# Kernel tuning notes

Measured on AMD Instinct MI355X. Metric: run time of the kernel, lower is better.

Reference implementation:

```python
import jax, jax.numpy as jnp
import numpy as np

DT = 0.01
B = 2097152
STATE_DIM, LATENT_DIM, INPUT_DIM = 3, 4, 3
TOTAL = STATE_DIM + LATENT_DIM  # 7
HID_L, HID_B = 64, 32


def setup_inputs() -> dict:
    key = jax.random.key(0)
    ks = jax.random.split(key, 16)
    def w(k, shape, fan_in):
        return (jax.random.normal(k, shape, dtype=jnp.float32) / np.sqrt(fan_in)).astype(jnp.float32)
    return {
        "state": jax.random.normal(ks[0], (B, TOTAL), dtype=jnp.float32),
        "u": jax.random.normal(ks[1], (B, INPUT_DIM), dtype=jnp.float32),
        # linear physics prior: s_dot = s@A.T + u@Bm.T ; y_phys = s@C.T
        "A": w(ks[2], (STATE_DIM, STATE_DIM), STATE_DIM),
        "Bm": w(ks[3], (STATE_DIM, INPUT_DIM), INPUT_DIM),
        "C": w(ks[4], (STATE_DIM, STATE_DIM), STATE_DIM),
        # z_gate: Linear(10 -> 7) + sigmoid
        "Wz": w(ks[5], (TOTAL, TOTAL + INPUT_DIM), TOTAL + INPUT_DIM),
        "bz": jnp.full((TOTAL,), 2.0, dtype=jnp.float32),
        # latent_dyn: Linear(10 -> 64) tanh Linear(64 -> 4)
        "W1": w(ks[6], (HID_L, TOTAL + INPUT_DIM), TOTAL + INPUT_DIM),
        "b1": jnp.zeros((HID_L,), dtype=jnp.float32),
        "W2": w(ks[7], (LATENT_DIM, HID_L), HID_L),
        "b2": jnp.zeros((LATENT_DIM,), dtype=jnp.float32),
        # 3 branches stacked: Linear(6 -> 32) tanh Linear(32 -> 1)
        "Wb1": w(ks[8], (3, HID_B, STATE_DIM + INPUT_DIM), STATE_DIM + INPUT_DIM),
        "bb1": jnp.zeros((3, HID_B), dtype=jnp.float32),
        "Wb2": w(ks[9], (3, HID_B), HID_B),
        "bb2": jnp.zeros((3,), dtype=jnp.float32),
    }


def reference(state, u, A, Bm, C, Wz, bz, W1, b1, W2, b2, Wb1, bb1, Wb2, bb2):
    s = state[:, :STATE_DIM]          # [B,3]
    latent = state[:, STATE_DIM:]     # [B,4]
    # physics prior
    s_dot_phys = s @ A.T + u @ Bm.T   # [B,3]
    y_phys = s @ C.T                  # [B,3]
    s_phys_next = s + DT * s_dot_phys
    su = jnp.concatenate([state, u], axis=1)  # [B,10]
    # latent dynamics
    latent_dot = jnp.tanh(su @ W1.T + b1) @ W2.T + b2   # [B,4]
    latent_next = latent + DT * latent_dot
    candidate = jnp.concatenate([s_phys_next, latent_next], axis=1)  # [B,7]
    # update gate
    z = jax.nn.sigmoid(su @ Wz.T + bz)                  # [B,7]
    next_state = z * candidate + (1.0 - z) * state
    # residual branch heads (vectorized over the 3 heads)
    branch_in = jnp.concatenate([s, u], axis=1)         # [B,6]
    h = jnp.tanh(jnp.einsum('bi,khi->bkh', branch_in, Wb1) + bb1)  # [B,3,32]
    residuals = jnp.einsum('bkh,kh->bk', h, Wb2) + bb2  # [B,3]
    y = y_phys + residuals
    return (next_state, y)
```

## Files before the change

kernel.cpp:

```cpp
#include <hip/hip_runtime.h>
#include <stdint.h>


#define DT_C  0.01f
#define NROWS 2097152
#define LOG2E 1.4426950408889634f
#define TBL_H   0.03125f
#define INV_H   32.0f
#define INV_H2  16.0f
#define TBL_C   256.0f
#define TBL_MAX 511.999f

typedef __fp16 h2 __attribute__((ext_vector_type(2)));

__device__ __forceinline__ h2 pkrtz(float a, float b) {
    return __builtin_amdgcn_cvt_pkrtz(a, b);
}

#if __has_builtin(__builtin_amdgcn_fdot2)
__device__ __forceinline__ float fdot2(h2 a, h2 b, float c) {
    return __builtin_amdgcn_fdot2(a, b, c, false);
}
#else
__device__ __forceinline__ float fdot2(h2 a, h2 b, float c) {
    return fmaf((float)a[0], (float)b[0], fmaf((float)a[1], (float)b[1], c));
}
#endif

__device__ __forceinline__ float tanh_ref(float x) {
    float e = __builtin_amdgcn_exp2f(x * (2.0f * LOG2E));
    return 1.0f - 2.0f * __builtin_amdgcn_rcpf(1.0f + e);
}

__device__ __forceinline__ float fract_f(float x) {
#if __has_builtin(__builtin_amdgcn_fractf)
    return __builtin_amdgcn_fractf(x);
#else
    return x - truncf(x);
#endif
}

__device__ __forceinline__ float med3f(float x, float lo, float hi) {
#if __has_builtin(__builtin_amdgcn_fmed3f)
    return __builtin_amdgcn_fmed3f(x, lo, hi);
#else
    return fminf(fmaxf(x, lo), hi);
#endif
}

__device__ __forceinline__ float tanh_lut(float t, const float2* lut) {
    float tc = med3f(t, 0.0f, TBL_MAX);
    float fr = fract_f(tc);
    int   i  = (int)tc;
    float2 e = lut[i];
    return fmaf(e.y, fr, e.x);
}

#define W1P_OFF   0
#define WZP_OFF   320
#define WB1P_OFF  355
#define W2P_OFF   643
#define PHYSP_OFF 771
#define CP_OFF    780
#define B1S_OFF   786
#define BZS_OFF   850
#define BB1S_OFF  857

__device__ __forceinline__ uint32_t pack2(float a, float b) {
    h2 v = pkrtz(a, b);
    uint32_t u; __builtin_memcpy(&u, &v, 4); return u;
}

__global__ void prep_kernel(const float* __restrict__ A, const float* __restrict__ Bm,
                            const float* __restrict__ C, const float* __restrict__ Wz,
                            const float* __restrict__ bz, const float* __restrict__ W1,
                            const float* __restrict__ b1, const float* __restrict__ Wb1,
                            const float* __restrict__ bb1, const float* __restrict__ W2,
                            uint32_t* __restrict__ ws)
{
    const int tid = blockIdx.x * blockDim.x + threadIdx.x;
    const int nt = gridDim.x * blockDim.x;
    float* wsf = (float*)ws;

    for (int i = tid; i < 320; i += nt) {
        int h = i / 5, j = i % 5;
        ws[W1P_OFF + i] = pack2(W1[h*10 + 2*j] * INV_H, W1[h*10 + 2*j + 1] * INV_H);
    }
    for (int i = tid; i < 35; i += nt) {
        int r = i / 5, j = i % 5;
        ws[WZP_OFF + i] = pack2(Wz[r*10 + 2*j] * INV_H2, Wz[r*10 + 2*j + 1] * INV_H2);
    }
    for (int i = tid; i < 288; i += nt) {
        int row = i / 3, j = i % 3;
        ws[WB1P_OFF + i] = pack2(Wb1[row*6 + 2*j] * INV_H, Wb1[row*6 + 2*j + 1] * INV_H);
    }
    for (int i = tid; i < 128; i += nt) {
        int k = i / 32, j = i % 32;
        ws[W2P_OFF + i] = pack2(W2[k*64 + 2*j], W2[k*64 + 2*j + 1]);
    }
    for (int i = tid; i < 9; i += nt) {
        int r = i / 3, j = i % 3;
        float a, b;
        if (j == 0) { a = A[r*3+0];  b = A[r*3+1];  }
        else if (j == 1) { a = A[r*3+2];  b = Bm[r*3+0]; }
        else { a = Bm[r*3+1]; b = Bm[r*3+2]; }
        ws[PHYSP_OFF + i] = pack2(a, b);
    }
    for (int i = tid; i < 6; i += nt) {
        int r = i / 2, j = i % 2;
        float a = (j == 0) ? C[r*3+0] : C[r*3+2];
        float b = (j == 0) ? C[r*3+1] : 0.0f;
        ws[CP_OFF + i] = pack2(a, b);
    }
    for (int i = tid; i < 64; i += nt) wsf[B1S_OFF + i] = fmaf(b1[i], INV_H, TBL_C);
    for (int i = tid; i < 7;  i += nt) wsf[BZS_OFF + i] = fmaf(bz[i], INV_H2, TBL_C);
    for (int i = tid; i < 96; i += nt) wsf[BB1S_OFF + i] = fmaf(bb1[i], INV_H, TBL_C);
}

__global__ __launch_bounds__(256) void phygru_kernel(
    const float* __restrict__ state, const float* __restrict__ u,
    const uint32_t* __restrict__ ws, const float* __restrict__ b2,
    const float* __restrict__ Wb2,   const float* __restrict__ bb2,
    float* __restrict__ out)
{
    __shared__ float2 lut[512];
    {
        const int t0 = threadIdx.x;
        #pragma unroll
        for (int r = 0; r < 2; ++r) {
            int j = t0 + r * 256;
            float x  = (j - 256) * TBL_H;
            float v0 = tanh_ref(x);
            float v1 = tanh_ref(x + TBL_H);
            lut[j] = make_float2(v0, v1 - v0);
        }
    }
    __syncthreads();

    const int row = blockIdx.x * blockDim.x + threadIdx.x;

    const h2* W1p  = (const h2*)(ws + W1P_OFF);
    const h2* Wzp  = (const h2*)(ws + WZP_OFF);
    const h2* Wb1p = (const h2*)(ws + WB1P_OFF);
    const h2* W2p  = (const h2*)(ws + W2P_OFF);
    const h2* Pp   = (const h2*)(ws + PHYSP_OFF);
    const h2* Cp   = (const h2*)(ws + CP_OFF);
    const float* wsf  = (const float*)ws;
    const float* b1s  = wsf + B1S_OFF;
    const float* bzs  = wsf + BZS_OFF;
    const float* bb1s = wsf + BB1S_OFF;

    float st[7];
    #pragma unroll
    for (int i = 0; i < 7; ++i) st[i] = state[row * 7 + i];
    float uu[3];
    #pragma unroll
    for (int i = 0; i < 3; ++i) uu[i] = u[row * 3 + i];

    h2 suh[5];
    suh[0] = pkrtz(st[0], st[1]);
    suh[1] = pkrtz(st[2], st[3]);
    suh[2] = pkrtz(st[4], st[5]);
    suh[3] = pkrtz(st[6], uu[0]);
    suh[4] = pkrtz(uu[1], uu[2]);
    h2 bih[3];
    bih[0] = suh[0];
    bih[1] = pkrtz(st[2], uu[0]);
    bih[2] = suh[4];

    float sp[3], yp[3];
    #pragma unroll
    for (int r = 0; r < 3; ++r) {
        float sd = fdot2(Pp[r*3+0], bih[0],
                   fdot2(Pp[r*3+1], bih[1],
                   fdot2(Pp[r*3+2], bih[2], 0.0f)));
        sp[r] = fmaf(DT_C, sd, st[r]);
        yp[r] = fdot2(Cp[r*2+0], bih[0], fdot2(Cp[r*2+1], bih[1], 0.0f));
    }

    float ld0 = b2[0], ld1 = b2[1], ld2 = b2[2], ld3 = b2[3];
    #pragma unroll
    for (int hp = 0; hp < 32; ++hp) {
        const int h0 = 2 * hp, h1 = 2 * hp + 1;
        float a0 = b1s[h0], a1 = b1s[h1];
        #pragma unroll
        for (int j = 0; j < 5; ++j) {
            a0 = fdot2(W1p[h0*5 + j], suh[j], a0);
            a1 = fdot2(W1p[h1*5 + j], suh[j], a1);
        }
        h2 th = pkrtz(tanh_lut(a0, lut), tanh_lut(a1, lut));
        ld0 = fdot2(W2p[0*32 + hp], th, ld0);
        ld1 = fdot2(W2p[1*32 + hp], th, ld1);
        ld2 = fdot2(W2p[2*32 + hp], th, ld2);
        ld3 = fdot2(W2p[3*32 + hp], th, ld3);
    }
    float ln[4];
    ln[0] = fmaf(DT_C, ld0, st[3]);
    ln[1] = fmaf(DT_C, ld1, st[4]);
    ln[2] = fmaf(DT_C, ld2, st[5]);
    ln[3] = fmaf(DT_C, ld3, st[6]);

    float ns[7];
    #pragma unroll
    for (int j = 0; j < 7; ++j) {
        float a = bzs[j];
        #pragma unroll
        for (int i = 0; i < 5; ++i) a = fdot2(Wzp[j*5 + i], suh[i], a);
        float z = fmaf(0.5f, tanh_lut(a, lut), 0.5f);
        float cand = (j < 3) ? sp[j] : ln[j - 3];
        ns[j] = fmaf(z, cand - st[j], st[j]);
    }

    float res[3];
    #pragma unroll
    for (int k = 0; k < 3; ++k) {
        float r = bb2[k];
        #pragma unroll
        for (int h = 0; h < 32; ++h) {
            float a = bb1s[k*32 + h];
            #pragma unroll
            for (int j = 0; j < 3; ++j)
                a = fdot2(Wb1p[(k*32 + h)*3 + j], bih[j], a);
            r = fmaf(Wb2[k*32 + h], tanh_lut(a, lut), r);
        }
        res[k] = r;
    }

    #pragma unroll
    for (int j = 0; j < 7; ++j) out[row * 7 + j] = ns[j];
    float* yout = out + (size_t)NROWS * 7;
    #pragma unroll
    for (int k = 0; k < 3; ++k) yout[row * 3 + k] = yp[k] + res[k];
}

extern "C" void kernel_launch(void* const* d_in, const int* in_sizes, int n_in,
                              void* d_out, int out_size, void* d_ws, size_t ws_size,
                              hipStream_t stream) {
    const float* state = (const float*)d_in[0];
    const float* u     = (const float*)d_in[1];
    const float* A     = (const float*)d_in[2];
    const float* Bm    = (const float*)d_in[3];
    const float* C     = (const float*)d_in[4];
    const float* Wz    = (const float*)d_in[5];
    const float* bz    = (const float*)d_in[6];
    const float* W1    = (const float*)d_in[7];
    const float* b1    = (const float*)d_in[8];
    const float* W2    = (const float*)d_in[9];
    const float* b2    = (const float*)d_in[10];
    const float* Wb1   = (const float*)d_in[11];
    const float* bb1   = (const float*)d_in[12];
    const float* Wb2   = (const float*)d_in[13];
    const float* bb2   = (const float*)d_in[14];
    float* out = (float*)d_out;
    uint32_t* ws = (uint32_t*)d_ws;

    prep_kernel<<<4, 256, 0, stream>>>(A, Bm, C, Wz, bz, W1, b1, Wb1, bb1, W2, ws);
    phygru_kernel<<<NROWS / 256, 256, 0, stream>>>(state, u, ws, b2, Wb2, bb2, out);
}
```

Measured before the change: 250.1 us.

## Process two rows per thread to amortize weight loads and LUT setup

Each thread now handles two consecutive rows, so every weight scalar load (uniform, via SMEM/constant path) and every bias read is shared across both rows, and the grid is halved. This also halves the per-block LUT construction and barrier overhead relative to work done. In exchange, register pressure roughly doubles for the live state, which may reduce occupancy, and the per-thread loads and stores become a stride of 14 and 6 floats, which is less coalesced.

```diff
diff --git a/kernel.cpp b/kernel.cpp
--- a/kernel.cpp
+++ b/kernel.cpp
@@ -137,7 +137,7 @@
     }
     __syncthreads();
 
-    const int row = blockIdx.x * blockDim.x + threadIdx.x;
+    const int tid = blockIdx.x * blockDim.x + threadIdx.x;
 
     const h2* W1p  = (const h2*)(ws + W1P_OFF);
     const h2* Wzp  = (const h2*)(ws + WZP_OFF);
@@ -150,87 +150,125 @@
     const float* bzs  = wsf + BZS_OFF;
     const float* bb1s = wsf + BB1S_OFF;
 
-    float st[7];
-    #pragma unroll
-    for (int i = 0; i < 7; ++i) st[i] = state[row * 7 + i];
-    float uu[3];
-    #pragma unroll
-    for (int i = 0; i < 3; ++i) uu[i] = u[row * 3 + i];
-
-    h2 suh[5];
-    suh[0] = pkrtz(st[0], st[1]);
-    suh[1] = pkrtz(st[2], st[3]);
-    suh[2] = pkrtz(st[4], st[5]);
-    suh[3] = pkrtz(st[6], uu[0]);
-    suh[4] = pkrtz(uu[1], uu[2]);
-    h2 bih[3];
-    bih[0] = suh[0];
-    bih[1] = pkrtz(st[2], uu[0]);
-    bih[2] = suh[4];
-
-    float sp[3], yp[3];
-    #pragma unroll
-    for (int r = 0; r < 3; ++r) {
-        float sd = fdot2(Pp[r*3+0], bih[0],
-                   fdot2(Pp[r*3+1], bih[1],
-                   fdot2(Pp[r*3+2], bih[2], 0.0f)));
-        sp[r] = fmaf(DT_C, sd, st[r]);
-        yp[r] = fdot2(Cp[r*2+0], bih[0], fdot2(Cp[r*2+1], bih[1], 0.0f));
-    }
-
-    float ld0 = b2[0], ld1 = b2[1], ld2 = b2[2], ld3 = b2[3];
+    float st[2][7], uu[2][3];
+    {
+        const float* sb = state + (size_t)tid * 14;
+        #pragma unroll
+        for (int r = 0; r < 2; ++r)
+            #pragma unroll
+            for (int i = 0; i < 7; ++i) st[r][i] = sb[r * 7 + i];
+        const float* ub = u + (size_t)tid * 6;
+        #pragma unroll
+        for (int r = 0; r < 2; ++r)
+            #pragma unroll
+            for (int i = 0; i < 3; ++i) uu[r][i] = ub[r * 3 + i];
+    }
+
+    h2 suh[2][5], bih[2][3];
+    #pragma unroll
+    for (int r = 0; r < 2; ++r) {
+        suh[r][0] = pkrtz(st[r][0], st[r][1]);
+        suh[r][1] = pkrtz(st[r][2], st[r][3]);
+        suh[r][2] = pkrtz(st[r][4], st[r][5]);
+        suh[r][3] = pkrtz(st[r][6], uu[r][0]);
+        suh[r][4] = pkrtz(uu[r][1], uu[r][2]);
+        bih[r][0] = suh[r][0];
+        bih[r][1] = pkrtz(st[r][2], uu[r][0]);
+        bih[r][2] = suh[r][4];
+    }
+
+    float sp[2][3], yp[2][3];
+    #pragma unroll
+    for (int r = 0; r < 2; ++r)
+        #pragma unroll
+        for (int q = 0; q < 3; ++q) {
+            float sd = fdot2(Pp[q*3+0], bih[r][0],
+                       fdot2(Pp[q*3+1], bih[r][1],
+                       fdot2(Pp[q*3+2], bih[r][2], 0.0f)));
+            sp[r][q] = fmaf(DT_C, sd, st[r][q]);
+            yp[r][q] = fdot2(Cp[q*2+0], bih[r][0], fdot2(Cp[q*2+1], bih[r][1], 0.0f));
+        }
+
+    float ld[2][4];
+    #pragma unroll
+    for (int r = 0; r < 2; ++r) {
+        ld[r][0] = b2[0]; ld[r][1] = b2[1]; ld[r][2] = b2[2]; ld[r][3] = b2[3];
+    }
     #pragma unroll
     for (int hp = 0; hp < 32; ++hp) {
         const int h0 = 2 * hp, h1 = 2 * hp + 1;
-        float a0 = b1s[h0], a1 = b1s[h1];
+        float a0_0 = b1s[h0], a1_0 = b1s[h1];
+        float a0_1 = b1s[h0], a1_1 = b1s[h1];
         #pragma unroll
         for (int j = 0; j < 5; ++j) {
-            a0 = fdot2(W1p[h0*5 + j], suh[j], a0);
-            a1 = fdot2(W1p[h1*5 + j], suh[j], a1);
-        }
-        h2 th = pkrtz(tanh_lut(a0, lut), tanh_lut(a1, lut));
-        ld0 = fdot2(W2p[0*32 + hp], th, ld0);
-        ld1 = fdot2(W2p[1*32 + hp], th, ld1);
-        ld2 = fdot2(W2p[2*32 + hp], th, ld2);
-        ld3 = fdot2(W2p[3*32 + hp], th, ld3);
-    }
-    float ln[4];
-    ln[0] = fmaf(DT_C, ld0, st[3]);
-    ln[1] = fmaf(DT_C, ld1, st[4]);
-    ln[2] = fmaf(DT_C, ld2, st[5]);
-    ln[3] = fmaf(DT_C, ld3, st[6]);
-
-    float ns[7];
+            a0_0 = fdot2(W1p[h0*5 + j], suh[0][j], a0_0);
+            a0_1 = fdot2(W1p[h0*5 + j], suh[1][j], a0_1);
+            a1_0 = fdot2(W1p[h1*5 + j], suh[0][j], a1_0);
+            a1_1 = fdot2(W1p[h1*5 + j], suh[1][j], a1_1);
+        }
+        h2 th0 = pkrtz(tanh_lut(a0_0, lut), tanh_lut(a1_0, lut));
+        h2 th1 = pkrtz(tanh_lut(a0_1, lut), tanh_lut(a1_1, lut));
+        #pragma unroll
+        for (int k = 0; k < 4; ++k) {
+            ld[0][k] = fdot2(W2p[k*32 + hp], th0, ld[0][k]);
+            ld[1][k] = fdot2(W2p[k*32 + hp], th1, ld[1][k]);
+        }
+    }
+    float ln[2][4];
+    #pragma unroll
+    for (int r = 0; r < 2; ++r)
+        #pragma unroll
+        for (int k = 0; k < 4; ++k)
+            ln[r][k] = fmaf(DT_C, ld[r][k], st[r][3 + k]);
+
+    float ns[2][7];
     #pragma unroll
     for (int j = 0; j < 7; ++j) {
-        float a = bzs[j];
-        #pragma unroll
-        for (int i = 0; i < 5; ++i) a = fdot2(Wzp[j*5 + i], suh[i], a);
-        float z = fmaf(0.5f, tanh_lut(a, lut), 0.5f);
-        float cand = (j < 3) ? sp[j] : ln[j - 3];
-        ns[j] = fmaf(z, cand - st[j], st[j]);
-    }
-
-    float res[3];
+        float a_0 = bzs[j], a_1 = bzs[j];
+        #pragma unroll
+        for (int i = 0; i < 5; ++i) {
+            a_0 = fdot2(Wzp[j*5 + i], suh[0][i], a_0);
+            a_1 = fdot2(Wzp[j*5 + i], suh[1][i], a_1);
+        }
+        float z0 = fmaf(0.5f, tanh_lut(a_0, lut), 0.5f);
+        float z1 = fmaf(0.5f, tanh_lut(a_1, lut), 0.5f);
+        float c0 = (j < 3) ? sp[0][j] : ln[0][j - 3];
+        float c1 = (j < 3) ? sp[1][j] : ln[1][j - 3];
+        ns[0][j] = fmaf(z0, c0 - st[0][j], st[0][j]);
+        ns[1][j] = fmaf(z1, c1 - st[1][j], st[1][j]);
+    }
+
+    float res[2][3];
     #pragma unroll
     for (int k = 0; k < 3; ++k) {
-        float r = bb2[k];
+        float r0 = bb2[k], r1 = bb2[k];
         #pragma unroll
         for (int h = 0; h < 32; ++h) {
-            float a = bb1s[k*32 + h];
-            #pragma unroll
-            for (int j = 0; j < 3; ++j)
-                a = fdot2(Wb1p[(k*32 + h)*3 + j], bih[j], a);
-            r = fmaf(Wb2[k*32 + h], tanh_lut(a, lut), r);
-        }
-        res[k] = r;
-    }
-
-    #pragma unroll
-    for (int j = 0; j < 7; ++j) out[row * 7 + j] = ns[j];
-    float* yout = out + (size_t)NROWS * 7;
-    #pragma unroll
-    for (int k = 0; k < 3; ++k) yout[row * 3 + k] = yp[k] + res[k];
+            float a_0 = bb1s[k*32 + h], a_1 = a_0;
+            #pragma unroll
+            for (int j = 0; j < 3; ++j) {
+                a_0 = fdot2(Wb1p[(k*32 + h)*3 + j], bih[0][j], a_0);
+                a_1 = fdot2(Wb1p[(k*32 + h)*3 + j], bih[1][j], a_1);
+            }
+            float w = Wb2[k*32 + h];
+            r0 = fmaf(w, tanh_lut(a_0, lut), r0);
+            r1 = fmaf(w, tanh_lut(a_1, lut), r1);
+        }
+        res[0][k] = r0; res[1][k] = r1;
+    }
+
+    {
+        float* ob = out + (size_t)tid * 14;
+        #pragma unroll
+        for (int r = 0; r < 2; ++r)
+            #pragma unroll
+            for (int j = 0; j < 7; ++j) ob[r * 7 + j] = ns[r][j];
+        float* yb = out + (size_t)NROWS * 7 + (size_t)tid * 6;
+        #pragma unroll
+        for (int r = 0; r < 2; ++r)
+            #pragma unroll
+            for (int k = 0; k < 3; ++k) yb[r * 3 + k] = yp[r][k] + res[r][k];
+    }
 }
 
 extern "C" void kernel_launch(void* const* d_in, const int* in_sizes, int n_in,
@@ -255,5 +293,5 @@
     uint32_t* ws = (uint32_t*)d_ws;
 
     prep_kernel<<<4, 256, 0, stream>>>(A, Bm, C, Wz, bz, W1, b1, Wb1, bb1, W2, ws);
-    phygru_kernel<<<NROWS / 256, 256, 0, stream>>>(state, u, ws, b2, Wb2, bb2, out);
-}
+    phygru_kernel<<<NROWS / 512, 256, 0, stream>>>(state, u, ws, b2, Wb2, bb2, out);
+}
```

Result: slower. 276.2 us (+10.4%).
